# Kernel optimization log

Measured on AMD Instinct MI355X. Metric: run time of the kernel, lower is better.

## Reference

```python
import jax, jax.numpy as jnp
import numpy as np

EMBED_DIM = 512
NUM_HEADS = 8
HEAD_DIM = EMBED_DIM // NUM_HEADS


def setup_inputs() -> dict:
    key = jax.random.key(0)
    ks = jax.random.split(key, 9)
    s = 1.0 / np.sqrt(EMBED_DIM)
    x = jax.random.normal(ks[0], (2, 4096, EMBED_DIM), dtype=jnp.float32)
    return {
        "x": x,
        "Wq": jax.random.uniform(ks[1], (EMBED_DIM, EMBED_DIM), jnp.float32, -s, s),
        "bq": jax.random.uniform(ks[2], (EMBED_DIM,), jnp.float32, -s, s),
        "Wk": jax.random.uniform(ks[3], (EMBED_DIM, EMBED_DIM), jnp.float32, -s, s),
        "bk": jax.random.uniform(ks[4], (EMBED_DIM,), jnp.float32, -s, s),
        "Wv": jax.random.uniform(ks[5], (EMBED_DIM, EMBED_DIM), jnp.float32, -s, s),
        "bv": jax.random.uniform(ks[6], (EMBED_DIM,), jnp.float32, -s, s),
        "Wo": jax.random.uniform(ks[7], (EMBED_DIM, EMBED_DIM), jnp.float32, -s, s),
        "bo": jax.random.uniform(ks[8], (EMBED_DIM,), jnp.float32, -s, s),
    }


def reference(x, Wq, bq, Wk, bk, Wv, bv, Wo, bo):
    B, S, E = x.shape
    H, D = NUM_HEADS, HEAD_DIM
    # projections (torch Linear: x @ W.T + b)
    q = (x @ Wq.T + bq).reshape(B, S, H, D).transpose(0, 2, 1, 3)  # [B,H,S,D]
    k = (x @ Wk.T + bk).reshape(B, S, H, D).transpose(0, 2, 1, 3)
    v = (x @ Wv.T + bv).reshape(B, S, H, D).transpose(0, 2, 1, 3)
    scores = jnp.einsum("bhsd,bhtd->bhst", q, k) / np.sqrt(D)  # [B,H,S,S]
    attn = jax.nn.softmax(scores, axis=-1)
    out = jnp.einsum("bhst,bhtd->bhsd", attn, v)  # [B,H,S,D]
    out = out.transpose(0, 2, 1, 3).reshape(B, S, E)
    return out @ Wo.T + bo + x
```

## Files before the change

kernel.cpp:

```cpp
#include <hip/hip_runtime.h>
#include <hip/hip_bf16.h>


typedef __attribute__((ext_vector_type(8))) short short8;
typedef __attribute__((ext_vector_type(4))) short short4v;
typedef __attribute__((ext_vector_type(4))) float floatx4;
typedef __attribute__((ext_vector_type(2))) float floatx2;

#define SEQ 4096
#define EMB 512
#define NH 8
#define HD 64
#define MROWS 8192
#define SC2 0.18033688011112042f

__device__ inline unsigned short f2bf_rne(float f) {
    union { float f; unsigned int u; } c; c.f = f;
    unsigned int u = c.u;
    return (unsigned short)((u + 0x7FFFu + ((u >> 16) & 1u)) >> 16);
}

__device__ inline short8 load8f(const float* __restrict__ p) {
    float4 a = *(const float4*)p;
    float4 b = *(const float4*)(p + 4);
    short8 r;
    r[0] = (short)f2bf_rne(a.x); r[1] = (short)f2bf_rne(a.y);
    r[2] = (short)f2bf_rne(a.z); r[3] = (short)f2bf_rne(a.w);
    r[4] = (short)f2bf_rne(b.x); r[5] = (short)f2bf_rne(b.y);
    r[6] = (short)f2bf_rne(b.z); r[7] = (short)f2bf_rne(b.w);
    return r;
}

__device__ inline void gload_lds16(const unsigned short* g, unsigned short* l) {
    __builtin_amdgcn_global_load_lds(
        (__attribute__((address_space(1))) void*)(void*)g,
        (__attribute__((address_space(3))) void*)l,
        16, 0, 0);
}

__device__ inline unsigned int pk_bf2(float a, float b) {
    union { float f; unsigned int u; } ca, cb; ca.f = a; cb.f = b;
    return __builtin_amdgcn_perm(cb.u + 0x8000u, ca.u + 0x8000u, 0x07060302u);
}

__device__ inline unsigned int pk_bf2t(float a, float b) {
    union { float f; unsigned int u; } ca, cb; ca.f = a; cb.f = b;
    return __builtin_amdgcn_perm(cb.u, ca.u, 0x07060302u);
}

__global__ __launch_bounds__(256) void convert_kernel(
    const float* __restrict__ x, const float* __restrict__ Wq,
    const float* __restrict__ Wk, const float* __restrict__ Wv,
    const float* __restrict__ Wo, unsigned short* __restrict__ xb,
    unsigned short* __restrict__ wb)
{
    const size_t i8 = ((size_t)blockIdx.x * 256 + threadIdx.x) * 8;
    const float* src; unsigned short* dst;
    if (i8 < (size_t)MROWS * EMB) { src = x + i8; dst = xb + i8; }
    else {
        size_t j = i8 - (size_t)MROWS * EMB;
        int w = (int)(j >> 18); size_t off = j & 262143;
        src = (w == 0 ? Wq : w == 1 ? Wk : w == 2 ? Wv : Wo) + off;
        dst = wb + (size_t)w * 262144 + off;
    }
    *(short8*)dst = load8f(src);
}

__global__ __launch_bounds__(256) void qkv_kernel(
    const unsigned short* __restrict__ xb, const unsigned short* __restrict__ wb,
    const float* __restrict__ bq, const float* __restrict__ bk,
    const float* __restrict__ bv, unsigned short* __restrict__ Qo,
    unsigned short* __restrict__ Ko, unsigned short* __restrict__ VTo)
{
    __shared__ unsigned short smem[32768];

    const int tid = threadIdx.x, wave = tid >> 6, lane = tid & 63;
    const int quad = lane >> 4, l16 = lane & 15;
    const int wm = wave >> 1, wn = wave & 1;
    const int row0 = blockIdx.x * 128, col0 = blockIdx.y * 128;
    const int z = blockIdx.z;

    unsigned short* sA = smem;
    unsigned short* sB = smem + 16384;

    const unsigned short* A = xb + (size_t)row0 * EMB;
    const unsigned short* Bm = wb + (size_t)z * 262144 + (size_t)col0 * EMB;
    const float* bias = z == 0 ? bq : z == 1 ? bk : bv;
    unsigned short* out = z == 0 ? Qo : z == 1 ? Ko : VTo;

    auto stage = [&](int buf, int k0) {
#pragma unroll
        for (int it = 0; it < 4; ++it) {
            const int s = it * 256 + tid;
            const int row = s >> 3, cg = (s & 7) ^ (row & 7);
            const size_t go = (size_t)row * EMB + k0 + cg * 8;
            gload_lds16(A + go, &sA[buf * 8192 + (it * 256 + wave * 64) * 8]);
            gload_lds16(Bm + go, &sB[buf * 8192 + (it * 256 + wave * 64) * 8]);
        }
    };

    floatx4 acc[4][4];
#pragma unroll
    for (int i = 0; i < 4; ++i)
#pragma unroll
        for (int j = 0; j < 4; ++j) { floatx4 zz = {0.f,0.f,0.f,0.f}; acc[i][j] = zz; }

    stage(0, 0);
    int buf = 0;
    for (int k0 = 0; k0 < EMB; k0 += 64) {
        __syncthreads();
        if (k0 + 64 < EMB) stage(buf ^ 1, k0 + 64);
#pragma unroll
        for (int kk = 0; kk < 2; ++kk) {
            short8 a[4], b[4];
#pragma unroll
            for (int mi = 0; mi < 4; ++mi)
                a[mi] = *(const short8*)&sA[buf * 8192 + (wm * 64 + mi * 16 + l16) * 64 + (((kk * 4 + quad) ^ (l16 & 7)) << 3)];
#pragma unroll
            for (int ni = 0; ni < 4; ++ni)
                b[ni] = *(const short8*)&sB[buf * 8192 + (wn * 64 + ni * 16 + l16) * 64 + (((kk * 4 + quad) ^ (l16 & 7)) << 3)];
            if (z != 2) {
#pragma unroll
                for (int i = 0; i < 4; ++i)
#pragma unroll
                    for (int j = 0; j < 4; ++j)
                        acc[i][j] = __builtin_amdgcn_mfma_f32_16x16x32_bf16(b[i], a[j], acc[i][j], 0, 0, 0);
            } else {
#pragma unroll
                for (int i = 0; i < 4; ++i)
#pragma unroll
                    for (int j = 0; j < 4; ++j)
                        acc[i][j] = __builtin_amdgcn_mfma_f32_16x16x32_bf16(a[i], b[j], acc[i][j], 0, 0, 0);
            }
        }
        buf ^= 1;
    }

    __syncthreads();
    unsigned short* ct = smem;
    const float qs = (z == 0) ? SC2 : 1.0f;
    if (z != 2) {
#pragma unroll
        for (int i = 0; i < 4; ++i) {
            const int n0 = wn * 64 + i * 16 + quad * 4;
            const float4 fb = *(const float4*)&bias[col0 + n0];
#pragma unroll
            for (int j = 0; j < 4; ++j) {
                const int m = wm * 64 + j * 16 + l16;
                ushort4 pk;
                pk.x = f2bf_rne((acc[i][j][0] + fb.x) * qs);
                pk.y = f2bf_rne((acc[i][j][1] + fb.y) * qs);
                pk.z = f2bf_rne((acc[i][j][2] + fb.z) * qs);
                pk.w = f2bf_rne((acc[i][j][3] + fb.w) * qs);
                *(ushort4*)&ct[m * 132 + n0] = pk;
            }
        }
    } else {
#pragma unroll
        for (int j = 0; j < 4; ++j) {
            const int n = wn * 64 + j * 16 + l16;
            const float fb = bias[col0 + n];
#pragma unroll
            for (int i = 0; i < 4; ++i) {
                const int m0 = wm * 64 + i * 16 + quad * 4;
                ushort4 pk;
                pk.x = f2bf_rne(acc[i][j][0] + fb);
                pk.y = f2bf_rne(acc[i][j][1] + fb);
                pk.z = f2bf_rne(acc[i][j][2] + fb);
                pk.w = f2bf_rne(acc[i][j][3] + fb);
                *(ushort4*)&ct[n * 132 + m0] = pk;
            }
        }
    }
    __syncthreads();
#pragma unroll
    for (int it = 0; it < 8; ++it) {
        const int idx = it * 256 + tid;
        const int row = idx >> 4, chunk = idx & 15;
        short8 v = *(const short8*)&ct[row * 132 + chunk * 8];
        size_t addr;
        if (z != 2) {
            const int m_g = row0 + row;
            const int b = m_g >> 12, s = m_g & 4095;
            const int n_g = col0 + chunk * 8;
            const int h = n_g >> 6, d = n_g & 63;
            addr = ((size_t)((b * NH + h) * SEQ + s)) * HD + d;
        } else {
            const int n_g = col0 + row;
            const int h = n_g >> 6, d = n_g & 63;
            const int m_g = row0 + chunk * 8;
            const int b = m_g >> 12, s0 = m_g & 4095;
            addr = ((size_t)((b * NH + h) * HD + d)) * SEQ + s0;
        }
        *(short8*)&out[addr] = v;
    }
}

__global__ __launch_bounds__(256, 2) void attn_kernel(
    const unsigned short* __restrict__ Q, const unsigned short* __restrict__ K,
    const unsigned short* __restrict__ VT, unsigned short* __restrict__ Oout)
{
    __shared__ unsigned short smem[32768];
    __shared__ float sPS[256];

    const int tid = threadIdx.x, wave = tid >> 6, lane = tid & 63;
    const int quad = lane >> 4, l16 = lane & 15;
    const int bh = blockIdx.x, q0 = blockIdx.y * 64;
    const int xm = l16 & 7;

    const unsigned short* Qh = Q + (size_t)bh * SEQ * HD;
    const unsigned short* Kh = K + (size_t)bh * SEQ * HD;
    const unsigned short* Vh = VT + (size_t)bh * HD * SEQ;

    short8 qf[4][2];
#pragma unroll
    for (int mi = 0; mi < 4; ++mi)
#pragma unroll
        for (int kk = 0; kk < 2; ++kk)
            qf[mi][kk] = *(const short8*)(Qh + (size_t)(q0 + mi * 16 + l16) * HD + kk * 32 + quad * 8);

    int kbase[2], kx0[2], kx1[2];
#pragma unroll
    for (int T = 0; T < 2; ++T) {
        const int R = wave * 32 + ((l16 >> 2) << 3) + (T << 2) + (l16 & 3);
        const int fR = (R & 7) ^ ((R >> 2) & 7);
        kbase[T] = R * 64;
        kx0[T] = (quad ^ fR) << 3;
        kx1[T] = ((4 + quad) ^ fR) << 3;
    }

    floatx4 oacc[4][4];
#pragma unroll
    for (int mi = 0; mi < 4; ++mi)
#pragma unroll
        for (int dt = 0; dt < 4; ++dt) { floatx4 zz = {0.f,0.f,0.f,0.f}; oacc[mi][dt] = zz; }
    floatx4 sacc[4];
#pragma unroll
    for (int mi = 0; mi < 4; ++mi) { floatx4 zz = {0.f,0.f,0.f,0.f}; sacc[mi] = zz; }
    const floatx4 z4 = {0.f, 0.f, 0.f, 0.f};
    const short ob = (short)0x3F80;
    const short8 ones8 = {ob, ob, ob, ob, ob, ob, ob, ob};

    auto stage = [&](int buf, int t0) {
        unsigned short* sK  = &smem[buf * 16384];
        unsigned short* sVT = &smem[buf * 16384 + 8192];
#pragma unroll
        for (int it = 0; it < 4; ++it) {
            const int s = it * 256 + tid;
            const int rK = s >> 3, jK = s & 7;
            const int cK = jK ^ ((rK & 7) ^ ((rK >> 2) & 7));
            gload_lds16(Kh + (size_t)(t0 + rK) * HD + cK * 8, &sK[(it * 256 + wave * 64) * 8]);
            const int rV = s >> 4, jV = s & 15;
            const int cV = jV ^ (rV & 7);
            gload_lds16(Vh + (size_t)rV * SEQ + t0 + cV * 8, &sVT[(it * 256 + wave * 64) * 8]);
        }
    };

    stage(0, 0);
    int buf = 0;
    for (int t0 = 0; t0 < SEQ; t0 += 128) {
        __syncthreads();
        if (t0 + 128 < SEQ) stage(buf ^ 1, t0 + 128);

        const unsigned short* sKs  = &smem[buf * 16384];
        const unsigned short* sVTs = &smem[buf * 16384 + 8192];

        short8 bK0[2], bK1[2];
#pragma unroll
        for (int T = 0; T < 2; ++T) {
            bK0[T] = *(const short8*)&sKs[kbase[T] + kx0[T]];
            bK1[T] = *(const short8*)&sKs[kbase[T] + kx1[T]];
        }
        short8 bv8[4];
#pragma unroll
        for (int dt = 0; dt < 4; ++dt)
            bv8[dt] = *(const short8*)&sVTs[(dt * 16 + l16) * 128 + (((wave * 4 + quad) ^ xm) << 3)];

#pragma unroll
        for (int mi = 0; mi < 4; ++mi) {
            floatx4 s0 = __builtin_amdgcn_mfma_f32_16x16x32_bf16(bK0[0], qf[mi][0], z4, 0, 0, 0);
            floatx4 s1 = __builtin_amdgcn_mfma_f32_16x16x32_bf16(bK0[1], qf[mi][0], z4, 0, 0, 0);
            s0 = __builtin_amdgcn_mfma_f32_16x16x32_bf16(bK1[0], qf[mi][1], s0, 0, 0, 0);
            s1 = __builtin_amdgcn_mfma_f32_16x16x32_bf16(bK1[1], qf[mi][1], s1, 0, 0, 0);

            float e0 = __builtin_amdgcn_exp2f(s0[0]);
            float e1 = __builtin_amdgcn_exp2f(s0[1]);
            float e2 = __builtin_amdgcn_exp2f(s0[2]);
            float e3 = __builtin_amdgcn_exp2f(s0[3]);
            float e4 = __builtin_amdgcn_exp2f(s1[0]);
            float e5 = __builtin_amdgcn_exp2f(s1[1]);
            float e6 = __builtin_amdgcn_exp2f(s1[2]);
            float e7 = __builtin_amdgcn_exp2f(s1[3]);
            union { uint4 u; short8 s; } cv;
            cv.u.x = pk_bf2t(e0, e1);
            cv.u.y = pk_bf2t(e2, e3);
            cv.u.z = pk_bf2t(e4, e5);
            cv.u.w = pk_bf2t(e6, e7);
            const short8 paf = cv.s;

            sacc[mi] = __builtin_amdgcn_mfma_f32_16x16x32_bf16(paf, ones8, sacc[mi], 0, 0, 0);
#pragma unroll
            for (int dt = 0; dt < 4; ++dt)
                oacc[mi][dt] = __builtin_amdgcn_mfma_f32_16x16x32_bf16(paf, bv8[dt], oacc[mi][dt], 0, 0, 0);
        }
        buf ^= 1;
    }

    if (l16 == 0) {
#pragma unroll
        for (int mi = 0; mi < 4; ++mi)
#pragma unroll
            for (int r = 0; r < 4; ++r)
                sPS[wave * 64 + mi * 16 + quad * 4 + r] = sacc[mi][r];
    }

    float* sRed = (float*)smem;
    const int b = bh >> 3, h = bh & 7;
    const int qr = wave * 16 + l16;

#pragma unroll
    for (int hh = 0; hh < 2; ++hh) {
        __syncthreads();
#pragma unroll
        for (int mi = 0; mi < 4; ++mi)
#pragma unroll
            for (int dd = 0; dd < 2; ++dd)
#pragma unroll
                for (int r = 0; r < 4; ++r)
                    sRed[wave * 2176 + (mi * 16 + quad * 4 + r) * 34 + dd * 16 + l16] =
                        oacc[mi][hh * 2 + dd][r];
        __syncthreads();
        floatx2 o8[4] = {{0.f,0.f},{0.f,0.f},{0.f,0.f},{0.f,0.f}};
#pragma unroll
        for (int w2 = 0; w2 < 4; ++w2) {
            const float* base = &sRed[w2 * 2176 + qr * 34 + quad * 8];
#pragma unroll
            for (int p = 0; p < 4; ++p) {
                floatx2 v = *(const floatx2*)(base + p * 2);
                o8[p] += v;
            }
        }
        const float pst = sPS[qr] + sPS[64 + qr] + sPS[128 + qr] + sPS[192 + qr];
        const float inv = 1.0f / pst;
        union { uint4 u; short8 s; } pk;
        pk.u.x = pk_bf2(o8[0][0] * inv, o8[0][1] * inv);
        pk.u.y = pk_bf2(o8[1][0] * inv, o8[1][1] * inv);
        pk.u.z = pk_bf2(o8[2][0] * inv, o8[2][1] * inv);
        pk.u.w = pk_bf2(o8[3][0] * inv, o8[3][1] * inv);
        const size_t addr = ((size_t)b * SEQ + q0 + qr) * EMB + h * HD + hh * 32 + quad * 8;
        *(short8*)&Oout[addr] = pk.s;
    }
}

__global__ __launch_bounds__(256) void outproj_kernel(
    const unsigned short* __restrict__ Ain, const unsigned short* __restrict__ wob,
    const float* __restrict__ bias, const float* __restrict__ X,
    float* __restrict__ out)
{
    __shared__ unsigned short sA[2][4096];
    __shared__ unsigned short sB[2][8192];

    const int tid = threadIdx.x, wave = tid >> 6, lane = tid & 63;
    const int quad = lane >> 4, l16 = lane & 15;
    const int wm = wave >> 1, wn = wave & 1;
    const int row0 = blockIdx.x * 64, col0 = blockIdx.y * 128;

    const unsigned short* A = Ain + (size_t)row0 * EMB;
    const unsigned short* Bm = wob + (size_t)col0 * EMB;

    auto stage = [&](int buf, int k0) {
#pragma unroll
        for (int it = 0; it < 2; ++it) {
            const int s = it * 256 + tid;
            const int row = s >> 3, cg = (s & 7) ^ (row & 7);
            gload_lds16(A + (size_t)row * EMB + k0 + cg * 8, &sA[buf][(it * 256 + wave * 64) * 8]);
        }
#pragma unroll
        for (int it = 0; it < 4; ++it) {
            const int s = it * 256 + tid;
            const int row = s >> 3, cg = (s & 7) ^ (row & 7);
            gload_lds16(Bm + (size_t)row * EMB + k0 + cg * 8, &sB[buf][(it * 256 + wave * 64) * 8]);
        }
    };

    floatx4 acc[2][4];
#pragma unroll
    for (int mi = 0; mi < 2; ++mi)
#pragma unroll
        for (int ni = 0; ni < 4; ++ni) { floatx4 zz = {0.f,0.f,0.f,0.f}; acc[mi][ni] = zz; }

    stage(0, 0);
    int buf = 0;
    for (int k0 = 0; k0 < EMB; k0 += 64) {
        __syncthreads();
        if (k0 + 64 < EMB) stage(buf ^ 1, k0 + 64);
#pragma unroll
        for (int kk = 0; kk < 2; ++kk) {
            short8 a[2], b[4];
#pragma unroll
            for (int mi = 0; mi < 2; ++mi)
                a[mi] = *(const short8*)&sA[buf][(wm * 32 + mi * 16 + l16) * 64 + (((kk * 4 + quad) ^ (l16 & 7)) << 3)];
#pragma unroll
            for (int ni = 0; ni < 4; ++ni)
                b[ni] = *(const short8*)&sB[buf][(wn * 64 + ni * 16 + l16) * 64 + (((kk * 4 + quad) ^ (l16 & 7)) << 3)];
#pragma unroll
            for (int mi = 0; mi < 2; ++mi)
#pragma unroll
                for (int ni = 0; ni < 4; ++ni)
                    acc[mi][ni] = __builtin_amdgcn_mfma_f32_16x16x32_bf16(a[mi], b[ni], acc[mi][ni], 0, 0, 0);
        }
        buf ^= 1;
    }

#pragma unroll
    for (int mi = 0; mi < 2; ++mi)
#pragma unroll
        for (int ni = 0; ni < 4; ++ni) {
            const int n = col0 + wn * 64 + ni * 16 + l16;
            const float bs = bias[n];
#pragma unroll
            for (int r = 0; r < 4; ++r) {
                const int m = row0 + wm * 32 + mi * 16 + quad * 4 + r;
                const size_t idx = (size_t)m * EMB + n;
                out[idx] = acc[mi][ni][r] + bs + X[idx];
            }
        }
}

extern "C" void kernel_launch(void* const* d_in, const int* in_sizes, int n_in,
                              void* d_out, int out_size, void* d_ws, size_t ws_size,
                              hipStream_t stream) {
    const float* x  = (const float*)d_in[0];
    const float* Wq = (const float*)d_in[1];
    const float* bq = (const float*)d_in[2];
    const float* Wk = (const float*)d_in[3];
    const float* bk = (const float*)d_in[4];
    const float* Wv = (const float*)d_in[5];
    const float* bv = (const float*)d_in[6];
    const float* Wo = (const float*)d_in[7];
    const float* bo = (const float*)d_in[8];
    float* out = (float*)d_out;

    const size_t SZ = (size_t)MROWS * EMB;
    unsigned short* wsXB = (unsigned short*)d_ws;
    unsigned short* wsWB = wsXB + SZ;
    unsigned short* wsQ  = wsWB + 4 * 262144;
    unsigned short* wsK  = wsQ + SZ;
    unsigned short* wsVT = wsK + SZ;

    convert_kernel<<<2560, 256, 0, stream>>>(x, Wq, Wk, Wv, Wo, wsXB, wsWB);
    qkv_kernel<<<dim3(MROWS / 128, EMB / 128, 3), 256, 0, stream>>>(
        wsXB, wsWB, bq, bk, bv, wsQ, wsK, wsVT);
    attn_kernel<<<dim3(2 * NH, SEQ / 64), 256, 0, stream>>>(wsQ, wsK, wsVT, wsXB);
    outproj_kernel<<<dim3(MROWS / 64, EMB / 128), 256, 0, stream>>>(
        wsXB, wsWB + 3 * 262144, bo, x, out);
}
```

Before: 198.2 us.

## Split attention waves into 2 query groups x 2 key halves with 64-key tiles

The attention block now covers 128 queries, with waves arranged as two query groups and two key-split halves instead of four key-split waves over 64 queries. Each K/V tile drops to 64 keys, so the LDS footprint halves, and the final reduction merges only two partial accumulators through shared memory. The launch grid halves. The epilogue now writes scalar bf16 stores instead of 16-byte vector stores, and there are fewer blocks to fill the GPU.

```diff
diff --git a/kernel.cpp b/kernel.cpp
--- a/kernel.cpp
+++ b/kernel.cpp
@@ -200,12 +200,13 @@
     const unsigned short* __restrict__ Q, const unsigned short* __restrict__ K,
     const unsigned short* __restrict__ VT, unsigned short* __restrict__ Oout)
 {
-    __shared__ unsigned short smem[32768];
-    __shared__ float sPS[256];
+    __shared__ unsigned short smem[16384];
+    __shared__ float sPS2[128];
 
     const int tid = threadIdx.x, wave = tid >> 6, lane = tid & 63;
     const int quad = lane >> 4, l16 = lane & 15;
-    const int bh = blockIdx.x, q0 = blockIdx.y * 64;
+    const int wq = wave >> 1, wt = wave & 1;
+    const int bh = blockIdx.x, q0 = blockIdx.y * 128;
     const int xm = l16 & 7;
 
     const unsigned short* Qh = Q + (size_t)bh * SEQ * HD;
@@ -217,12 +218,12 @@
     for (int mi = 0; mi < 4; ++mi)
 #pragma unroll
         for (int kk = 0; kk < 2; ++kk)
-            qf[mi][kk] = *(const short8*)(Qh + (size_t)(q0 + mi * 16 + l16) * HD + kk * 32 + quad * 8);
+            qf[mi][kk] = *(const short8*)(Qh + (size_t)(q0 + wq * 64 + mi * 16 + l16) * HD + kk * 32 + quad * 8);
 
     int kbase[2], kx0[2], kx1[2];
 #pragma unroll
     for (int T = 0; T < 2; ++T) {
-        const int R = wave * 32 + ((l16 >> 2) << 3) + (T << 2) + (l16 & 3);
+        const int R = wt * 32 + ((l16 >> 2) << 3) + (T << 2) + (l16 & 3);
         const int fR = (R & 7) ^ ((R >> 2) & 7);
         kbase[T] = R * 64;
         kx0[T] = (quad ^ fR) << 3;
@@ -242,28 +243,27 @@
     const short8 ones8 = {ob, ob, ob, ob, ob, ob, ob, ob};
 
     auto stage = [&](int buf, int t0) {
-        unsigned short* sK  = &smem[buf * 16384];
-        unsigned short* sVT = &smem[buf * 16384 + 8192];
-#pragma unroll
-        for (int it = 0; it < 4; ++it) {
-            const int s = it * 256 + tid;
-            const int rK = s >> 3, jK = s & 7;
-            const int cK = jK ^ ((rK & 7) ^ ((rK >> 2) & 7));
-            gload_lds16(Kh + (size_t)(t0 + rK) * HD + cK * 8, &sK[(it * 256 + wave * 64) * 8]);
-            const int rV = s >> 4, jV = s & 15;
-            const int cV = jV ^ (rV & 7);
-            gload_lds16(Vh + (size_t)rV * SEQ + t0 + cV * 8, &sVT[(it * 256 + wave * 64) * 8]);
+#pragma unroll
+        for (int psi = 0; psi < 2; ++psi) {
+            const int r = psi * 32 + wave * 8 + (lane >> 3);
+            const int j = lane & 7;
+            const int cK = j ^ ((r & 7) ^ ((r >> 2) & 7));
+            const int cV = j ^ (r & 7);
+            gload_lds16(Kh + (size_t)(t0 + r) * HD + cK * 8,
+                        &smem[buf * 4096 + psi * 2048 + wave * 512]);
+            gload_lds16(Vh + (size_t)r * SEQ + t0 + cV * 8,
+                        &smem[8192 + buf * 4096 + psi * 2048 + wave * 512]);
         }
     };
 
     stage(0, 0);
     int buf = 0;
-    for (int t0 = 0; t0 < SEQ; t0 += 128) {
+    for (int t0 = 0; t0 < SEQ; t0 += 64) {
         __syncthreads();
-        if (t0 + 128 < SEQ) stage(buf ^ 1, t0 + 128);
-
-        const unsigned short* sKs  = &smem[buf * 16384];
-        const unsigned short* sVTs = &smem[buf * 16384 + 8192];
+        if (t0 + 64 < SEQ) stage(buf ^ 1, t0 + 64);
+
+        const unsigned short* sKs  = &smem[buf * 4096];
+        const unsigned short* sVTs = &smem[8192 + buf * 4096];
 
         short8 bK0[2], bK1[2];
 #pragma unroll
@@ -274,7 +274,7 @@
         short8 bv8[4];
 #pragma unroll
         for (int dt = 0; dt < 4; ++dt)
-            bv8[dt] = *(const short8*)&sVTs[(dt * 16 + l16) * 128 + (((wave * 4 + quad) ^ xm) << 3)];
+            bv8[dt] = *(const short8*)&sVTs[(dt * 16 + l16) * 64 + (((wt * 4 + quad) ^ xm) << 3)];
 
 #pragma unroll
         for (int mi = 0; mi < 4; ++mi) {
@@ -283,14 +283,14 @@
             s0 = __builtin_amdgcn_mfma_f32_16x16x32_bf16(bK1[0], qf[mi][1], s0, 0, 0, 0);
             s1 = __builtin_amdgcn_mfma_f32_16x16x32_bf16(bK1[1], qf[mi][1], s1, 0, 0, 0);
 
-            float e0 = __builtin_amdgcn_exp2f(s0[0]);
-            float e1 = __builtin_amdgcn_exp2f(s0[1]);
-            float e2 = __builtin_amdgcn_exp2f(s0[2]);
-            float e3 = __builtin_amdgcn_exp2f(s0[3]);
-            float e4 = __builtin_amdgcn_exp2f(s1[0]);
-            float e5 = __builtin_amdgcn_exp2f(s1[1]);
-            float e6 = __builtin_amdgcn_exp2f(s1[2]);
-            float e7 = __builtin_amdgcn_exp2f(s1[3]);
+            const float e0 = __builtin_amdgcn_exp2f(s0[0]);
+            const float e1 = __builtin_amdgcn_exp2f(s0[1]);
+            const float e2 = __builtin_amdgcn_exp2f(s0[2]);
+            const float e3 = __builtin_amdgcn_exp2f(s0[3]);
+            const float e4 = __builtin_amdgcn_exp2f(s1[0]);
+            const float e5 = __builtin_amdgcn_exp2f(s1[1]);
+            const float e6 = __builtin_amdgcn_exp2f(s1[2]);
+            const float e7 = __builtin_amdgcn_exp2f(s1[3]);
             union { uint4 u; short8 s; } cv;
             cv.u.x = pk_bf2t(e0, e1);
             cv.u.y = pk_bf2t(e2, e3);
@@ -306,49 +306,42 @@
         buf ^= 1;
     }
 
-    if (l16 == 0) {
-#pragma unroll
-        for (int mi = 0; mi < 4; ++mi)
+    __syncthreads();
+    float* sRed = (float*)smem;
+    if (wt == 1) {
+#pragma unroll
+        for (int mi = 0; mi < 4; ++mi) {
+#pragma unroll
+            for (int dt = 0; dt < 4; ++dt)
+#pragma unroll
+                for (int r = 0; r < 4; ++r)
+                    sRed[wq * 4096 + (mi * 4 + dt) * 256 + (quad * 4 + r) * 16 + l16] = oacc[mi][dt][r];
+            if (l16 == 0) {
+#pragma unroll
+                for (int r = 0; r < 4; ++r)
+                    sPS2[wq * 64 + mi * 16 + quad * 4 + r] = sacc[mi][r];
+            }
+        }
+    }
+    __syncthreads();
+    if (wt == 0) {
+        const int b = bh >> 3, h = bh & 7;
+#pragma unroll
+        for (int mi = 0; mi < 4; ++mi) {
+            float inv[4];
 #pragma unroll
             for (int r = 0; r < 4; ++r)
-                sPS[wave * 64 + mi * 16 + quad * 4 + r] = sacc[mi][r];
-    }
-
-    float* sRed = (float*)smem;
-    const int b = bh >> 3, h = bh & 7;
-    const int qr = wave * 16 + l16;
-
-#pragma unroll
-    for (int hh = 0; hh < 2; ++hh) {
-        __syncthreads();
-#pragma unroll
-        for (int mi = 0; mi < 4; ++mi)
-#pragma unroll
-            for (int dd = 0; dd < 2; ++dd)
-#pragma unroll
-                for (int r = 0; r < 4; ++r)
-                    sRed[wave * 2176 + (mi * 16 + quad * 4 + r) * 34 + dd * 16 + l16] =
-                        oacc[mi][hh * 2 + dd][r];
-        __syncthreads();
-        floatx2 o8[4] = {{0.f,0.f},{0.f,0.f},{0.f,0.f},{0.f,0.f}};
-#pragma unroll
-        for (int w2 = 0; w2 < 4; ++w2) {
-            const float* base = &sRed[w2 * 2176 + qr * 34 + quad * 8];
-#pragma unroll
-            for (int p = 0; p < 4; ++p) {
-                floatx2 v = *(const floatx2*)(base + p * 2);
-                o8[p] += v;
-            }
-        }
-        const float pst = sPS[qr] + sPS[64 + qr] + sPS[128 + qr] + sPS[192 + qr];
-        const float inv = 1.0f / pst;
-        union { uint4 u; short8 s; } pk;
-        pk.u.x = pk_bf2(o8[0][0] * inv, o8[0][1] * inv);
-        pk.u.y = pk_bf2(o8[1][0] * inv, o8[1][1] * inv);
-        pk.u.z = pk_bf2(o8[2][0] * inv, o8[2][1] * inv);
-        pk.u.w = pk_bf2(o8[3][0] * inv, o8[3][1] * inv);
-        const size_t addr = ((size_t)b * SEQ + q0 + qr) * EMB + h * HD + hh * 32 + quad * 8;
-        *(short8*)&Oout[addr] = pk.s;
+                inv[r] = 1.0f / (sacc[mi][r] + sPS2[wq * 64 + mi * 16 + quad * 4 + r]);
+#pragma unroll
+            for (int dt = 0; dt < 4; ++dt)
+#pragma unroll
+                for (int r = 0; r < 4; ++r) {
+                    const float o = oacc[mi][dt][r] +
+                        sRed[wq * 4096 + (mi * 4 + dt) * 256 + (quad * 4 + r) * 16 + l16];
+                    const int s = q0 + wq * 64 + mi * 16 + quad * 4 + r;
+                    Oout[((size_t)b * SEQ + s) * EMB + h * HD + dt * 16 + l16] = f2bf_rne(o * inv[r]);
+                }
+        }
     }
 }
 
@@ -451,7 +444,7 @@
     convert_kernel<<<2560, 256, 0, stream>>>(x, Wq, Wk, Wv, Wo, wsXB, wsWB);
     qkv_kernel<<<dim3(MROWS / 128, EMB / 128, 3), 256, 0, stream>>>(
         wsXB, wsWB, bq, bk, bv, wsQ, wsK, wsVT);
-    attn_kernel<<<dim3(2 * NH, SEQ / 64), 256, 0, stream>>>(wsQ, wsK, wsVT, wsXB);
+    attn_kernel<<<dim3(2 * NH, SEQ / 128), 256, 0, stream>>>(wsQ, wsK, wsVT, wsXB);
     outproj_kernel<<<dim3(MROWS / 64, EMB / 128), 256, 0, stream>>>(
         wsXB, wsWB + 3 * 262144, bo, x, out);
 }
```

New measurement: 191.1 us. 3.6% less time.
